# Performance work log

Measured on AMD Instinct MI355X. Metric: run time of the kernel, lower is better.

The kernel has to match this reference:

```python
import jax, jax.numpy as jnp
import numpy as np

B, T, E, D, H = 8, 64, 4, 256, 1024  # batch, num_tokens, num_experts, hidden_dim, ffn_hidden_dim
SPARSITY_WEIGHT = 0.01


def setup_inputs() -> dict:
    key = jax.random.key(0)
    k_x, k_fc1, k_fc2, k_wr, k_br = jax.random.split(key, 5)
    x = jax.random.normal(k_x, (B, T, D), dtype=jnp.float32)
    # xavier_uniform per (t,e) slice: bound = sqrt(6/(fan_in+fan_out))
    a = float(np.sqrt(6.0 / (D + H)))
    fc1 = jax.random.uniform(k_fc1, (T, E, D, H), minval=-a, maxval=a, dtype=jnp.float32)
    b1 = jnp.zeros((T, E, H), dtype=jnp.float32)
    fc2 = jax.random.uniform(k_fc2, (T, E, H, D), minval=-a, maxval=a, dtype=jnp.float32)
    b2 = jnp.zeros((T, E, D), dtype=jnp.float32)
    # per-token routers (nn.Linear default init: U(-1/sqrt(D), 1/sqrt(D)))
    br_bound = float(1.0 / np.sqrt(D))
    Wr = jax.random.uniform(k_wr, (T, E, D), minval=-br_bound, maxval=br_bound, dtype=jnp.float32)
    br = jax.random.uniform(k_br, (T, E), minval=-br_bound, maxval=br_bound, dtype=jnp.float32)
    return {"x": x, "fc1": fc1, "b1": b1, "fc2": fc2, "b2": b2, "Wr": Wr, "br": br}


def reference(x, fc1, b1, fc2, b2, Wr, br):
    # x: [B,T,D]
    # ReLU routing gates per token/expert: [B,T,E]
    gates = jax.nn.relu(jnp.einsum('btd,ted->bte', x, Wr) + br)
    bsz = x.shape[0]
    aux_loss = SPARSITY_WEIGHT * gates.sum() / (bsz * x.shape[1])
    # Expert FFN, batched over (token, expert): hidden [B,T,E,H]
    hidden = jax.nn.gelu(jnp.einsum('btd,tedh->bteh', x, fc1) + b1, approximate=False)
    # dropout rate is 0.0 -> identity
    expert_out = jnp.einsum('bteh,tehd->bted', hidden, fc2) + b2  # [B,T,E,D]
    output = jnp.sum(expert_out * gates[..., None], axis=2)  # [B,T,D]
    return output, aux_loss
```

## Files before the change

### kernel.cpp

```cpp
#include <hip/hip_runtime.h>
#include <hip/hip_bf16.h>

namespace {

constexpr int kB = 8, kT = 64, kE = 4, kD = 256, kH = 1024;
constexpr int kNC = 4;
constexpr int kHc = kH / kNC;

__device__ __forceinline__ float gelu_exact(float v) {
  return 0.5f * v * (1.0f + erff(v * 0.70710678118654752f));
}

__global__ __launch_bounds__(256, 4)
void moe_ffn_kernel(const float* __restrict__ x,
                    const float* __restrict__ fc1,
                    const float* __restrict__ b1,
                    const float* __restrict__ fc2,
                    const float* __restrict__ b2,
                    const float* __restrict__ Wr,
                    const float* __restrict__ br,
                    float* __restrict__ out) {
  __shared__ float xs[kB][kD];
  __shared__ float hid[kB][kHc];
  __shared__ float gates_s[kB];

  const int tid = threadIdx.x;
  const int bid = blockIdx.x;
  const int te  = bid / kNC;
  const int c   = bid % kNC;
  const int t   = te >> 2;
  const int h0  = c * kHc;

#pragma unroll
  for (int b = 0; b < kB; ++b)
    xs[b][tid] = x[((size_t)b * kT + t) * kD + tid];
  __syncthreads();

  const int wave = tid >> 6, lane = tid & 63;

  {
    const float* __restrict__ wr = Wr + (size_t)te * kD;
    const float w0 = wr[lane], w1 = wr[lane + 64], w2 = wr[lane + 128], w3 = wr[lane + 192];
#pragma unroll
    for (int bb = 0; bb < 2; ++bb) {
      const int b = wave + bb * 4;
      float p = xs[b][lane] * w0 + xs[b][lane + 64] * w1 +
                xs[b][lane + 128] * w2 + xs[b][lane + 192] * w3;
#pragma unroll
      for (int off = 32; off; off >>= 1) p += __shfl_xor(p, off);
      if (lane == 0) {
        const float g = p + br[te];
        gates_s[b] = g > 0.0f ? g : 0.0f;
      }
    }
  }

  {
    const float* __restrict__ w = fc1 + (size_t)te * kD * kH + h0 + tid;
    float acc[kB] = {0.f, 0.f, 0.f, 0.f, 0.f, 0.f, 0.f, 0.f};
#pragma unroll 8
    for (int d = 0; d < kD; ++d) {
      const float wv = w[(size_t)d * kH];
#pragma unroll
      for (int b = 0; b < kB; ++b) acc[b] = fmaf(xs[b][d], wv, acc[b]);
    }
    const float bias = b1[(size_t)te * kH + h0 + tid];
#pragma unroll
    for (int b = 0; b < kB; ++b) hid[b][tid] = gelu_exact(acc[b] + bias);
  }
  __syncthreads();

  {
    const float* __restrict__ w = fc2 + (size_t)te * kH * kD + (size_t)h0 * kD + tid;
    float acc[kB] = {0.f, 0.f, 0.f, 0.f, 0.f, 0.f, 0.f, 0.f};
#pragma unroll 8
    for (int i = 0; i < kHc; ++i) {
      const float wv = w[(size_t)i * kD];
#pragma unroll
      for (int b = 0; b < kB; ++b) acc[b] = fmaf(hid[b][i], wv, acc[b]);
    }
    const float bias2 = (c == 0) ? b2[(size_t)te * kD + tid] : 0.f;
#pragma unroll
    for (int b = 0; b < kB; ++b)
      atomicAdd(&out[((size_t)b * kT + t) * kD + tid], gates_s[b] * (acc[b] + bias2));

    if (c == 0 && tid == 0) {
      float gs = 0.f;
#pragma unroll
      for (int b = 0; b < kB; ++b) gs += gates_s[b];
      atomicAdd(&out[(size_t)kB * kT * kD], 0.01f * gs * (1.0f / (kB * kT)));
    }
  }
}

}

extern "C" void kernel_launch(void* const* d_in, const int* in_sizes, int n_in,
                              void* d_out, int out_size, void* d_ws, size_t ws_size,
                              hipStream_t stream) {
  const float* x   = (const float*)d_in[0];
  const float* fc1 = (const float*)d_in[1];
  const float* b1  = (const float*)d_in[2];
  const float* fc2 = (const float*)d_in[3];
  const float* b2  = (const float*)d_in[4];
  const float* Wr  = (const float*)d_in[5];
  const float* br  = (const float*)d_in[6];
  float* out = (float*)d_out;

  hipMemsetAsync(d_out, 0, (size_t)out_size * sizeof(float), stream);

  moe_ffn_kernel<<<dim3(kT * kE * kNC), dim3(256), 0, stream>>>(x, fc1, b1, fc2, b2, Wr, br, out);
}
```

Before: 104.6 us.

## Split hidden dim into more chunks with 128-thread blocks and vectorized loads

Doubles the number of hidden-dimension chunks per (token, expert) and halves the block size to 128 threads, giving 2048 smaller blocks. x and hidden activations are read from shared memory as float4, and each thread computes two output columns in fc2 using float2 weight loads. The aim is more blocks in flight to hide the latency of the memory-bound weight streaming and fewer LDS instructions, at the cost of twice as many atomic adds to the output.

After: 115.9 us. 10.7% more time.

```diff
diff --git a/kernel.cpp b/kernel.cpp
--- a/kernel.cpp
+++ b/kernel.cpp
@@ -4,14 +4,15 @@
 namespace {
 
 constexpr int kB = 8, kT = 64, kE = 4, kD = 256, kH = 1024;
-constexpr int kNC = 4;
+constexpr int kNC = 8;
 constexpr int kHc = kH / kNC;
+constexpr int kThreads = 128;
 
 __device__ __forceinline__ float gelu_exact(float v) {
   return 0.5f * v * (1.0f + erff(v * 0.70710678118654752f));
 }
 
-__global__ __launch_bounds__(256, 4)
+__global__ __launch_bounds__(kThreads, 4)
 void moe_ffn_kernel(const float* __restrict__ x,
                     const float* __restrict__ fc1,
                     const float* __restrict__ b1,
@@ -31,9 +32,16 @@
   const int t   = te >> 2;
   const int h0  = c * kHc;
 
+  {
+    const float4* __restrict__ xsrc = reinterpret_cast<const float4*>(x);
+    float4* xdst = reinterpret_cast<float4*>(&xs[0][0]);
 #pragma unroll
-  for (int b = 0; b < kB; ++b)
-    xs[b][tid] = x[((size_t)b * kT + t) * kD + tid];
+    for (int i = 0; i < 4; ++i) {
+      const int f = i * kThreads + tid;
+      const int b = f >> 6, d4 = f & 63;
+      xdst[f] = xsrc[(size_t)(b * kT + t) * (kD / 4) + d4];
+    }
+  }
   __syncthreads();
 
   const int wave = tid >> 6, lane = tid & 63;
@@ -42,8 +50,8 @@
     const float* __restrict__ wr = Wr + (size_t)te * kD;
     const float w0 = wr[lane], w1 = wr[lane + 64], w2 = wr[lane + 128], w3 = wr[lane + 192];
 #pragma unroll
-    for (int bb = 0; bb < 2; ++bb) {
-      const int b = wave + bb * 4;
+    for (int bb = 0; bb < 4; ++bb) {
+      const int b = wave * 4 + bb;
       float p = xs[b][lane] * w0 + xs[b][lane + 64] * w1 +
                 xs[b][lane + 128] * w2 + xs[b][lane + 192] * w3;
 #pragma unroll
@@ -56,13 +64,25 @@
   }
 
   {
-    const float* __restrict__ w = fc1 + (size_t)te * kD * kH + h0 + tid;
+    const float* __restrict__ wp = fc1 + (size_t)te * kD * kH + h0 + tid;
     float acc[kB] = {0.f, 0.f, 0.f, 0.f, 0.f, 0.f, 0.f, 0.f};
-#pragma unroll 8
-    for (int d = 0; d < kD; ++d) {
-      const float wv = w[(size_t)d * kH];
+#pragma unroll 2
+    for (int d4 = 0; d4 < kD / 4; ++d4) {
+      float4 xv[kB];
 #pragma unroll
-      for (int b = 0; b < kB; ++b) acc[b] = fmaf(xs[b][d], wv, acc[b]);
+      for (int b = 0; b < kB; ++b)
+        xv[b] = *reinterpret_cast<const float4*>(&xs[b][d4 * 4]);
+      const float wa = wp[(size_t)(d4 * 4 + 0) * kH];
+      const float wb = wp[(size_t)(d4 * 4 + 1) * kH];
+      const float wc = wp[(size_t)(d4 * 4 + 2) * kH];
+      const float wd = wp[(size_t)(d4 * 4 + 3) * kH];
+#pragma unroll
+      for (int b = 0; b < kB; ++b) {
+        acc[b] = fmaf(xv[b].x, wa, acc[b]);
+        acc[b] = fmaf(xv[b].y, wb, acc[b]);
+        acc[b] = fmaf(xv[b].z, wc, acc[b]);
+        acc[b] = fmaf(xv[b].w, wd, acc[b]);
+      }
     }
     const float bias = b1[(size_t)te * kH + h0 + tid];
 #pragma unroll
@@ -71,19 +91,46 @@
   __syncthreads();
 
   {
-    const float* __restrict__ w = fc2 + (size_t)te * kH * kD + (size_t)h0 * kD + tid;
-    float acc[kB] = {0.f, 0.f, 0.f, 0.f, 0.f, 0.f, 0.f, 0.f};
-#pragma unroll 8
-    for (int i = 0; i < kHc; ++i) {
-      const float wv = w[(size_t)i * kD];
+    const float2* __restrict__ wp =
+        reinterpret_cast<const float2*>(fc2 + (size_t)te * kH * kD + (size_t)h0 * kD) + tid;
+    float2 acc2[kB];
 #pragma unroll
-      for (int b = 0; b < kB; ++b) acc[b] = fmaf(hid[b][i], wv, acc[b]);
+    for (int b = 0; b < kB; ++b) acc2[b] = make_float2(0.f, 0.f);
+#pragma unroll 2
+    for (int h4 = 0; h4 < kHc / 4; ++h4) {
+      float4 hv[kB];
+#pragma unroll
+      for (int b = 0; b < kB; ++b)
+        hv[b] = *reinterpret_cast<const float4*>(&hid[b][h4 * 4]);
+      const float2 wva = wp[(size_t)(h4 * 4 + 0) * (kD / 2)];
+      const float2 wvb = wp[(size_t)(h4 * 4 + 1) * (kD / 2)];
+      const float2 wvc = wp[(size_t)(h4 * 4 + 2) * (kD / 2)];
+      const float2 wvd = wp[(size_t)(h4 * 4 + 3) * (kD / 2)];
+#pragma unroll
+      for (int b = 0; b < kB; ++b) {
+        acc2[b].x = fmaf(hv[b].x, wva.x, acc2[b].x);
+        acc2[b].y = fmaf(hv[b].x, wva.y, acc2[b].y);
+        acc2[b].x = fmaf(hv[b].y, wvb.x, acc2[b].x);
+        acc2[b].y = fmaf(hv[b].y, wvb.y, acc2[b].y);
+        acc2[b].x = fmaf(hv[b].z, wvc.x, acc2[b].x);
+        acc2[b].y = fmaf(hv[b].z, wvc.y, acc2[b].y);
+        acc2[b].x = fmaf(hv[b].w, wvd.x, acc2[b].x);
+        acc2[b].y = fmaf(hv[b].w, wvd.y, acc2[b].y);
+      }
     }
-    const float bias2 = (c == 0) ? b2[(size_t)te * kD + tid] : 0.f;
+    const int d0 = 2 * tid;
+    float2 bias2 = make_float2(0.f, 0.f);
+    if (c == 0) {
+      bias2.x = b2[(size_t)te * kD + d0];
+      bias2.y = b2[(size_t)te * kD + d0 + 1];
+    }
 #pragma unroll
-    for (int b = 0; b < kB; ++b)
-      atomicAdd(&out[((size_t)b * kT + t) * kD + tid], gates_s[b] * (acc[b] + bias2));
-
+    for (int b = 0; b < kB; ++b) {
+      const float g = gates_s[b];
+      float* o = &out[((size_t)b * kT + t) * kD + d0];
+      atomicAdd(o,     g * (acc2[b].x + bias2.x));
+      atomicAdd(o + 1, g * (acc2[b].y + bias2.y));
+    }
     if (c == 0 && tid == 0) {
       float gs = 0.f;
 #pragma unroll
@@ -109,5 +156,6 @@
 
   hipMemsetAsync(d_out, 0, (size_t)out_size * sizeof(float), stream);
 
-  moe_ffn_kernel<<<dim3(kT * kE * kNC), dim3(256), 0, stream>>>(x, fc1, b1, fc2, b2, Wr, br, out);
+  moe_ffn_kernel<<<dim3(kT * kE * kNC), dim3(kThreads), 0, stream>>>(
+      x, fc1, b1, fc2, b2, Wr, br, out);
 }
```

## Split fused MoE FFN into two kernels with global hidden workspace

Applied to the files above, without the earlier changes.

When workspace is large enough, the single fused kernel is replaced by two launches. The first computes the GELU hidden activations for all (b,t,e) into global memory, and the second reads them back to compute FC2 plus the gating and atomic accumulation. Each FC2 block now covers a full 256-row chunk of H per (t,e), whereas before it used a 256-wide slice of its own FC1 output. This un-fuses the stages, adding a global round trip for the hidden tensor and an extra launch. It also drops the shared-memory staging of x and hidden, so those values are now read from global/L2 directly.

After: 159.0 us. +51.9%, slower.

```diff
diff --git a/kernel.cpp b/kernel.cpp
--- a/kernel.cpp
+++ b/kernel.cpp
@@ -4,22 +4,121 @@
 namespace {
 
 constexpr int kB = 8, kT = 64, kE = 4, kD = 256, kH = 1024;
+constexpr int kTE = kT * kE;
+constexpr size_t kHidElems = (size_t)kB * kTE * kH;
+
+__device__ __forceinline__ float gelu_exact(float v) {
+  return 0.5f * v * (1.0f + erff(v * 0.70710678118654752f));
+}
+
+__global__ __launch_bounds__(256, 4)
+void ffn1_kernel(const float* __restrict__ x,
+                 const float* __restrict__ fc1,
+                 const float* __restrict__ b1,
+                 float* __restrict__ hid) {
+  const int tid = threadIdx.x;
+  const int bid = blockIdx.x;
+  const int te  = bid >> 2;
+  const int c   = bid & 3;
+  const int t   = te >> 2;
+  const int h   = c * 256 + tid;
+
+  const float* __restrict__ wp = fc1 + (size_t)te * (kD * kH) + h;
+  const float* __restrict__ xp = x + (size_t)t * kD;
+
+  float acc[kB] = {0.f, 0.f, 0.f, 0.f, 0.f, 0.f, 0.f, 0.f};
+#pragma unroll 8
+  for (int d = 0; d < kD; ++d) {
+    const float wv = wp[(size_t)d * kH];
+#pragma unroll
+    for (int b = 0; b < kB; ++b) {
+      const float xv = xp[(size_t)b * (kT * kD) + d];
+      acc[b] = fmaf(xv, wv, acc[b]);
+    }
+  }
+  const float bias = b1[(size_t)te * kH + h];
+#pragma unroll
+  for (int b = 0; b < kB; ++b)
+    hid[((size_t)b * kTE + te) * kH + h] = gelu_exact(acc[b] + bias);
+}
+
+__global__ __launch_bounds__(256, 4)
+void ffn2_kernel(const float* __restrict__ x,
+                 const float* __restrict__ hid,
+                 const float* __restrict__ fc2,
+                 const float* __restrict__ b2,
+                 const float* __restrict__ Wr,
+                 const float* __restrict__ br,
+                 float* __restrict__ out) {
+  __shared__ float gates_s[kB];
+
+  const int tid = threadIdx.x;
+  const int bid = blockIdx.x;
+  const int te  = bid >> 2;
+  const int c   = bid & 3;
+  const int t   = te >> 2;
+
+  const int wave = tid >> 6, lane = tid & 63;
+
+  {
+    const float* __restrict__ wr = Wr + (size_t)te * kD;
+    const float w0 = wr[lane], w1 = wr[lane + 64], w2 = wr[lane + 128], w3 = wr[lane + 192];
+#pragma unroll
+    for (int bb = 0; bb < 2; ++bb) {
+      const int b = wave * 2 + bb;
+      const float* __restrict__ xb = x + ((size_t)b * kT + t) * kD;
+      float p = xb[lane] * w0 + xb[lane + 64] * w1 +
+                xb[lane + 128] * w2 + xb[lane + 192] * w3;
+#pragma unroll
+      for (int off = 32; off; off >>= 1) p += __shfl_xor(p, off);
+      if (lane == 0) {
+        const float g = p + br[te];
+        gates_s[b] = g > 0.0f ? g : 0.0f;
+      }
+    }
+  }
+  __syncthreads();
+
+  const int h0 = c * 256;
+  const float* __restrict__ wp = fc2 + (size_t)te * (kH * kD) + (size_t)h0 * kD + tid;
+  const float* __restrict__ hp = hid + (size_t)te * kH + h0;
+
+  float acc[kB] = {0.f, 0.f, 0.f, 0.f, 0.f, 0.f, 0.f, 0.f};
+#pragma unroll 8
+  for (int i = 0; i < 256; ++i) {
+    const float wv = wp[(size_t)i * kD];
+#pragma unroll
+    for (int b = 0; b < kB; ++b) {
+      const float hv = hp[(size_t)b * (kTE * kH) + i];
+      acc[b] = fmaf(hv, wv, acc[b]);
+    }
+  }
+
+  const float b2v = (c == 0) ? b2[(size_t)te * kD + tid] : 0.f;
+#pragma unroll
+  for (int b = 0; b < kB; ++b)
+    atomicAdd(&out[((size_t)b * kT + t) * kD + tid], gates_s[b] * (acc[b] + b2v));
+
+  if (c == 0 && tid == 0) {
+    float gs = 0.f;
+#pragma unroll
+    for (int b = 0; b < kB; ++b) gs += gates_s[b];
+    atomicAdd(&out[(size_t)kB * kT * kD], 0.01f * gs * (1.0f / (kB * kT)));
+  }
+}
+
 constexpr int kNC = 4;
 constexpr int kHc = kH / kNC;
 
-__device__ __forceinline__ float gelu_exact(float v) {
-  return 0.5f * v * (1.0f + erff(v * 0.70710678118654752f));
-}
-
 __global__ __launch_bounds__(256, 4)
-void moe_ffn_kernel(const float* __restrict__ x,
-                    const float* __restrict__ fc1,
-                    const float* __restrict__ b1,
-                    const float* __restrict__ fc2,
-                    const float* __restrict__ b2,
-                    const float* __restrict__ Wr,
-                    const float* __restrict__ br,
-                    float* __restrict__ out) {
+void moe_ffn_fused(const float* __restrict__ x,
+                   const float* __restrict__ fc1,
+                   const float* __restrict__ b1,
+                   const float* __restrict__ fc2,
+                   const float* __restrict__ b2,
+                   const float* __restrict__ Wr,
+                   const float* __restrict__ br,
+                   float* __restrict__ out) {
   __shared__ float xs[kB][kD];
   __shared__ float hid[kB][kHc];
   __shared__ float gates_s[kB];
@@ -37,7 +136,6 @@
   __syncthreads();
 
   const int wave = tid >> 6, lane = tid & 63;
-
   {
     const float* __restrict__ wr = Wr + (size_t)te * kD;
     const float w0 = wr[lane], w1 = wr[lane + 64], w2 = wr[lane + 128], w3 = wr[lane + 192];
@@ -109,5 +207,11 @@
 
   hipMemsetAsync(d_out, 0, (size_t)out_size * sizeof(float), stream);
 
-  moe_ffn_kernel<<<dim3(kT * kE * kNC), dim3(256), 0, stream>>>(x, fc1, b1, fc2, b2, Wr, br, out);
-}
+  if (ws_size >= kHidElems * sizeof(float)) {
+    float* hid = (float*)d_ws;
+    ffn1_kernel<<<dim3(kTE * 4), dim3(256), 0, stream>>>(x, fc1, b1, hid);
+    ffn2_kernel<<<dim3(kTE * 4), dim3(256), 0, stream>>>(x, hid, fc2, b2, Wr, br, out);
+  } else {
+    moe_ffn_fused<<<dim3(kTE * kNC), dim3(256), 0, stream>>>(x, fc1, b1, fc2, b2, Wr, br, out);
+  }
+}
```

## Split H into 8 chunks, split fc1 reduction over D across half-blocks, vectorize LDS reads

Applied to the files above, without the earlier changes.

Doubles the number of H-chunks per (token, expert) so twice as many blocks run, giving more memory-level parallelism for streaming the weights. In fc1, each 128-thread half of the block reduces over half of D, and the two partial sums are combined through shared memory before the GELU. Loads of x and shared-memory operands are widened to float4 so one LDS read feeds four FMAs. The cost is an extra barrier, twice as many atomicAdds into the output, and launch bounds raised to 8 blocks per unit, which tightens the register budget.

New measurement: 109.0 us. +4.1%, slower.

```diff
diff --git a/kernel.cpp b/kernel.cpp
--- a/kernel.cpp
+++ b/kernel.cpp
@@ -4,14 +4,14 @@
 namespace {
 
 constexpr int kB = 8, kT = 64, kE = 4, kD = 256, kH = 1024;
-constexpr int kNC = 4;
+constexpr int kNC = 8;
 constexpr int kHc = kH / kNC;
 
 __device__ __forceinline__ float gelu_exact(float v) {
   return 0.5f * v * (1.0f + erff(v * 0.70710678118654752f));
 }
 
-__global__ __launch_bounds__(256, 4)
+__global__ __launch_bounds__(256, 8)
 void moe_ffn_kernel(const float* __restrict__ x,
                     const float* __restrict__ fc1,
                     const float* __restrict__ b1,
@@ -26,14 +26,21 @@
 
   const int tid = threadIdx.x;
   const int bid = blockIdx.x;
-  const int te  = bid / kNC;
-  const int c   = bid % kNC;
+  const int te  = bid >> 3;
+  const int c   = bid & 7;
   const int t   = te >> 2;
   const int h0  = c * kHc;
 
+  {
+    const float4* __restrict__ xsrc = reinterpret_cast<const float4*>(x);
+    float4* xdst = reinterpret_cast<float4*>(&xs[0][0]);
 #pragma unroll
-  for (int b = 0; b < kB; ++b)
-    xs[b][tid] = x[((size_t)b * kT + t) * kD + tid];
+    for (int i = 0; i < 2; ++i) {
+      const int f = i * 256 + tid;
+      const int b = f >> 6, d4 = f & 63;
+      xdst[f] = xsrc[(size_t)(b * kT + t) * (kD / 4) + d4];
+    }
+  }
   __syncthreads();
 
   const int wave = tid >> 6, lane = tid & 63;
@@ -43,7 +50,7 @@
     const float w0 = wr[lane], w1 = wr[lane + 64], w2 = wr[lane + 128], w3 = wr[lane + 192];
 #pragma unroll
     for (int bb = 0; bb < 2; ++bb) {
-      const int b = wave + bb * 4;
+      const int b = wave * 2 + bb;
       float p = xs[b][lane] * w0 + xs[b][lane + 64] * w1 +
                 xs[b][lane + 128] * w2 + xs[b][lane + 192] * w3;
 #pragma unroll
@@ -55,34 +62,79 @@
     }
   }
 
+  const int half = tid >> 7;
+  const int hl   = tid & 127;
+  float acc[kB] = {0.f, 0.f, 0.f, 0.f, 0.f, 0.f, 0.f, 0.f};
   {
-    const float* __restrict__ w = fc1 + (size_t)te * kD * kH + h0 + tid;
-    float acc[kB] = {0.f, 0.f, 0.f, 0.f, 0.f, 0.f, 0.f, 0.f};
-#pragma unroll 8
-    for (int d = 0; d < kD; ++d) {
-      const float wv = w[(size_t)d * kH];
+    const float* __restrict__ wp = fc1 + (size_t)te * (kD * kH) + h0 + hl;
+    const int dbase = half * 128;
+#pragma unroll 2
+    for (int d4 = 0; d4 < 32; ++d4) {
+      const int d = dbase + d4 * 4;
+      const float w0 = wp[(size_t)(d + 0) * kH];
+      const float w1 = wp[(size_t)(d + 1) * kH];
+      const float w2 = wp[(size_t)(d + 2) * kH];
+      const float w3 = wp[(size_t)(d + 3) * kH];
 #pragma unroll
-      for (int b = 0; b < kB; ++b) acc[b] = fmaf(xs[b][d], wv, acc[b]);
+      for (int bg = 0; bg < 2; ++bg) {
+        float4 xv[4];
+#pragma unroll
+        for (int j = 0; j < 4; ++j)
+          xv[j] = *reinterpret_cast<const float4*>(&xs[bg * 4 + j][d]);
+#pragma unroll
+        for (int j = 0; j < 4; ++j) {
+          const int b = bg * 4 + j;
+          acc[b] = fmaf(xv[j].x, w0, acc[b]);
+          acc[b] = fmaf(xv[j].y, w1, acc[b]);
+          acc[b] = fmaf(xv[j].z, w2, acc[b]);
+          acc[b] = fmaf(xv[j].w, w3, acc[b]);
+        }
+      }
     }
-    const float bias = b1[(size_t)te * kH + h0 + tid];
+  }
+  if (half == 1) {
 #pragma unroll
-    for (int b = 0; b < kB; ++b) hid[b][tid] = gelu_exact(acc[b] + bias);
+    for (int b = 0; b < kB; ++b) hid[b][hl] = acc[b];
+  }
+  __syncthreads();
+  if (half == 0) {
+    const float bias = b1[(size_t)te * kH + h0 + hl];
+#pragma unroll
+    for (int b = 0; b < kB; ++b)
+      hid[b][hl] = gelu_exact(hid[b][hl] + acc[b] + bias);
   }
   __syncthreads();
 
   {
-    const float* __restrict__ w = fc2 + (size_t)te * kH * kD + (size_t)h0 * kD + tid;
-    float acc[kB] = {0.f, 0.f, 0.f, 0.f, 0.f, 0.f, 0.f, 0.f};
-#pragma unroll 8
-    for (int i = 0; i < kHc; ++i) {
-      const float wv = w[(size_t)i * kD];
+    const float* __restrict__ wp =
+        fc2 + (size_t)te * (kH * kD) + (size_t)h0 * kD + tid;
+    float acc2[kB] = {0.f, 0.f, 0.f, 0.f, 0.f, 0.f, 0.f, 0.f};
+#pragma unroll 2
+    for (int h4 = 0; h4 < 32; ++h4) {
+      const float w0 = wp[(size_t)(h4 * 4 + 0) * kD];
+      const float w1 = wp[(size_t)(h4 * 4 + 1) * kD];
+      const float w2 = wp[(size_t)(h4 * 4 + 2) * kD];
+      const float w3 = wp[(size_t)(h4 * 4 + 3) * kD];
 #pragma unroll
-      for (int b = 0; b < kB; ++b) acc[b] = fmaf(hid[b][i], wv, acc[b]);
+      for (int bg = 0; bg < 2; ++bg) {
+        float4 hv[4];
+#pragma unroll
+        for (int j = 0; j < 4; ++j)
+          hv[j] = *reinterpret_cast<const float4*>(&hid[bg * 4 + j][h4 * 4]);
+#pragma unroll
+        for (int j = 0; j < 4; ++j) {
+          const int b = bg * 4 + j;
+          acc2[b] = fmaf(hv[j].x, w0, acc2[b]);
+          acc2[b] = fmaf(hv[j].y, w1, acc2[b]);
+          acc2[b] = fmaf(hv[j].z, w2, acc2[b]);
+          acc2[b] = fmaf(hv[j].w, w3, acc2[b]);
+        }
+      }
     }
-    const float bias2 = (c == 0) ? b2[(size_t)te * kD + tid] : 0.f;
+    const float b2v = (c == 0) ? b2[(size_t)te * kD + tid] : 0.f;
 #pragma unroll
     for (int b = 0; b < kB; ++b)
-      atomicAdd(&out[((size_t)b * kT + t) * kD + tid], gates_s[b] * (acc[b] + bias2));
+      atomicAdd(&out[((size_t)b * kT + t) * kD + tid], gates_s[b] * (acc2[b] + b2v));
 
     if (c == 0 && tid == 0) {
       float gs = 0.f;
@@ -109,5 +161,6 @@
 
   hipMemsetAsync(d_out, 0, (size_t)out_size * sizeof(float), stream);
 
-  moe_ffn_kernel<<<dim3(kT * kE * kNC), dim3(256), 0, stream>>>(x, fc1, b1, fc2, b2, Wr, br, out);
+  moe_ffn_kernel<<<dim3(kT * kE * kNC), dim3(256), 0, stream>>>(
+      x, fc1, b1, fc2, b2, Wr, br, out);
 }
```
